# Optimization experiments

Hardware: AMD Instinct MI355X
Metric: run time of the kernel (lower is better)

## Reference

```python
import jax, jax.numpy as jnp
import numpy as np

H = 1024
S = 32768

def setup_inputs() -> dict:
    key = jax.random.key(0)
    ks = jax.random.split(key, 6)
    scale = 1.0 / np.sqrt(H)
    return {
        "hidden": jax.random.normal(ks[0], (H,), dtype=jnp.float32),
        "encoder_states": jax.random.normal(ks[1], (S, H), dtype=jnp.float32),
        "W_lin": jax.random.normal(ks[2], (H, H), dtype=jnp.float32) * scale,
        "b_lin": jax.random.normal(ks[3], (H,), dtype=jnp.float32) * scale,
        "W_attn": jax.random.normal(ks[4], (H, H), dtype=jnp.float32) * scale,
        "b_attn": jax.random.normal(ks[5], (H,), dtype=jnp.float32) * scale,
    }

def reference(hidden, encoder_states, W_lin, b_lin, W_attn, b_attn):
    # hidden = self.linear(hidden)  (torch Linear: x @ W.T + b)
    h = jnp.dot(W_lin, hidden) + b_lin               # [H]
    # 'general' score: energy = attn(hidden); e_i = enc_i . energy
    energy = jnp.dot(W_attn, h) + b_attn             # [H]
    attn_energies = encoder_states @ energy          # [S]  (vectorized GEMV over all timesteps)
    return jax.nn.softmax(attn_energies, axis=0)[:, None]  # [S, 1]
```

## Files before the change

### kernel.cpp

```cpp
#include <hip/hip_runtime.h>
#include <math.h>

#define H 1024
#define S 32768

__device__ __forceinline__ float wave_reduce_sum(float v) {
    #pragma unroll
    for (int off = 32; off > 0; off >>= 1) v += __shfl_xor(v, off, 64);
    return v;
}

__global__ __launch_bounds__(256) void gemv_kernel(const float* __restrict__ W,
                                                   const float* __restrict__ x,
                                                   const float* __restrict__ b,
                                                   float* __restrict__ y) {
    __shared__ float xs[H];
    const int tid = threadIdx.x;
    reinterpret_cast<float4*>(xs)[tid] = reinterpret_cast<const float4*>(x)[tid];
    __syncthreads();

    const int wave = tid >> 6, lane = tid & 63;
    const int row = blockIdx.x * 4 + wave;
    const float4* Wr = reinterpret_cast<const float4*>(W + (size_t)row * H);
    const float4* xs4 = reinterpret_cast<const float4*>(xs);

    float acc = 0.f;
    #pragma unroll
    for (int k = 0; k < 4; ++k) {
        const int idx = k * 64 + lane;
        const float4 w = Wr[idx];
        const float4 e = xs4[idx];
        acc += w.x * e.x + w.y * e.y + w.z * e.z + w.w * e.w;
    }
    acc = wave_reduce_sum(acc);
    if (lane == 0) y[row] = acc + b[row];
}

__global__ __launch_bounds__(256) void scores_kernel(const float* __restrict__ enc,
                                                     const float* __restrict__ energy,
                                                     float* __restrict__ scores,
                                                     float* __restrict__ blockmax) {
    __shared__ float es[H];
    __shared__ float smax[4];
    const int tid = threadIdx.x;
    reinterpret_cast<float4*>(es)[tid] = reinterpret_cast<const float4*>(energy)[tid];
    __syncthreads();

    const int wave = tid >> 6, lane = tid & 63;
    const int row = blockIdx.x * 4 + wave;
    const float4* Er = reinterpret_cast<const float4*>(enc + (size_t)row * H);
    const float4* es4 = reinterpret_cast<const float4*>(es);

    float acc = 0.f;
    #pragma unroll
    for (int k = 0; k < 4; ++k) {
        const int idx = k * 64 + lane;
        const float4 w = Er[idx];
        const float4 e = es4[idx];
        acc += w.x * e.x + w.y * e.y + w.z * e.z + w.w * e.w;
    }
    acc = wave_reduce_sum(acc);
    if (lane == 0) { scores[row] = acc; smax[wave] = acc; }
    __syncthreads();
    if (tid == 0) {
        blockmax[blockIdx.x] = fmaxf(fmaxf(smax[0], smax[1]), fmaxf(smax[2], smax[3]));
    }
}

__global__ __launch_bounds__(1024) void softmax_reduce_kernel(const float* __restrict__ scores,
                                                              const float* __restrict__ blockmax,
                                                              int nbm,
                                                              float* __restrict__ stats) {
    __shared__ float red[1024];
    const int tid = threadIdx.x;

    float m = -INFINITY;
    for (int i = tid; i < nbm; i += 1024) m = fmaxf(m, blockmax[i]);
    red[tid] = m;
    __syncthreads();
    for (int s = 512; s > 0; s >>= 1) {
        if (tid < s) red[tid] = fmaxf(red[tid], red[tid + s]);
        __syncthreads();
    }
    m = red[0];
    __syncthreads();

    float sum = 0.f;
    for (int i = tid; i < S; i += 1024) sum += expf(scores[i] - m);
    red[tid] = sum;
    __syncthreads();
    for (int s = 512; s > 0; s >>= 1) {
        if (tid < s) red[tid] += red[tid + s];
        __syncthreads();
    }
    if (tid == 0) { stats[0] = m; stats[1] = 1.0f / red[0]; }
}

__global__ __launch_bounds__(256) void normalize_kernel(const float* __restrict__ scores,
                                                        const float* __restrict__ stats,
                                                        float* __restrict__ out) {
    const int i = blockIdx.x * 256 + threadIdx.x;
    const float m = stats[0], inv = stats[1];
    out[i] = expf(scores[i] - m) * inv;
}

extern "C" void kernel_launch(void* const* d_in, const int* in_sizes, int n_in,
                              void* d_out, int out_size, void* d_ws, size_t ws_size,
                              hipStream_t stream) {
    const float* hidden = (const float*)d_in[0];
    const float* enc    = (const float*)d_in[1];
    const float* W_lin  = (const float*)d_in[2];
    const float* b_lin  = (const float*)d_in[3];
    const float* W_attn = (const float*)d_in[4];
    const float* b_attn = (const float*)d_in[5];
    float* out = (float*)d_out;
    float* ws  = (float*)d_ws;

    float* scores   = ws;
    float* blockmax = ws + S;
    float* h        = ws + S + 8192;
    float* energy   = ws + S + 8192 + H;
    float* stats    = ws + S + 8192 + 2*H;

    const int nblk_scores = S / 4;

    gemv_kernel<<<H / 4, 256, 0, stream>>>(W_lin, hidden, b_lin, h);
    gemv_kernel<<<H / 4, 256, 0, stream>>>(W_attn, h, b_attn, energy);
    scores_kernel<<<nblk_scores, 256, 0, stream>>>(enc, energy, scores, blockmax);
    softmax_reduce_kernel<<<1, 1024, 0, stream>>>(scores, blockmax, nblk_scores, stats);
    normalize_kernel<<<S / 256, 256, 0, stream>>>(scores, stats, out);
}
```

Measured before the change: 221.4 us.

## Fuse scores, softmax reduction and normalization via last-block atomic counter

Merges the scores GEMV, the softmax statistics reduction and the normalization into one kernel. Each block computes four rows per wave, a local max and a rescaled exp-sum. The last block to finish, detected with an atomic counter reset by the first GEMV, combines the per-block statistics and writes the normalized output. This removes two kernel launches and the single-block pass that recomputed exp over all scores. The trade-off is that the final normalization runs on only one block of 256 threads, which serializes that tail.

```diff
diff --git a/kernel.cpp b/kernel.cpp
--- a/kernel.cpp
+++ b/kernel.cpp
@@ -3,6 +3,7 @@
 
 #define H 1024
 #define S 32768
+#define NB3 2048
 
 __device__ __forceinline__ float wave_reduce_sum(float v) {
     #pragma unroll
@@ -13,95 +14,126 @@
 __global__ __launch_bounds__(256) void gemv_kernel(const float* __restrict__ W,
                                                    const float* __restrict__ x,
                                                    const float* __restrict__ b,
-                                                   float* __restrict__ y) {
+                                                   float* __restrict__ y,
+                                                   unsigned int* counter) {
     __shared__ float xs[H];
     const int tid = threadIdx.x;
+    if (counter && blockIdx.x == 0 && tid == 0) *counter = 0u;
     reinterpret_cast<float4*>(xs)[tid] = reinterpret_cast<const float4*>(x)[tid];
     __syncthreads();
 
     const int wave = tid >> 6, lane = tid & 63;
     const int row = blockIdx.x * 4 + wave;
-    const float4* Wr = reinterpret_cast<const float4*>(W + (size_t)row * H);
+    const float4* Wr  = reinterpret_cast<const float4*>(W + (size_t)row * H);
     const float4* xs4 = reinterpret_cast<const float4*>(xs);
 
     float acc = 0.f;
     #pragma unroll
     for (int k = 0; k < 4; ++k) {
-        const int idx = k * 64 + lane;
-        const float4 w = Wr[idx];
-        const float4 e = xs4[idx];
+        const float4 w = Wr[k * 64 + lane];
+        const float4 e = xs4[k * 64 + lane];
         acc += w.x * e.x + w.y * e.y + w.z * e.z + w.w * e.w;
     }
     acc = wave_reduce_sum(acc);
     if (lane == 0) y[row] = acc + b[row];
 }
 
-__global__ __launch_bounds__(256) void scores_kernel(const float* __restrict__ enc,
-                                                     const float* __restrict__ energy,
-                                                     float* __restrict__ scores,
-                                                     float* __restrict__ blockmax) {
+__global__ __launch_bounds__(256) void scores_softmax_kernel(
+    const float* __restrict__ enc,
+    const float* __restrict__ energy,
+    float* __restrict__ scores,
+    float* __restrict__ blockmax,
+    float* __restrict__ blocksum,
+    unsigned int* __restrict__ counter,
+    float* __restrict__ out)
+{
     __shared__ float es[H];
-    __shared__ float smax[4];
+    __shared__ float redm[4], reds[4];
+    __shared__ unsigned int isLast;
+
     const int tid = threadIdx.x;
     reinterpret_cast<float4*>(es)[tid] = reinterpret_cast<const float4*>(energy)[tid];
     __syncthreads();
 
     const int wave = tid >> 6, lane = tid & 63;
-    const int row = blockIdx.x * 4 + wave;
-    const float4* Er = reinterpret_cast<const float4*>(enc + (size_t)row * H);
+    const int bid  = blockIdx.x;
     const float4* es4 = reinterpret_cast<const float4*>(es);
 
-    float acc = 0.f;
+    const int wrow0 = (bid * 4 + wave) * 4;
+    float sc[4];
+    float wmax = -INFINITY;
     #pragma unroll
-    for (int k = 0; k < 4; ++k) {
-        const int idx = k * 64 + lane;
-        const float4 w = Er[idx];
-        const float4 e = es4[idx];
-        acc += w.x * e.x + w.y * e.y + w.z * e.z + w.w * e.w;
+    for (int p = 0; p < 4; ++p) {
+        const float4* Er = reinterpret_cast<const float4*>(enc + (size_t)(wrow0 + p) * H);
+        float acc = 0.f;
+        #pragma unroll
+        for (int k = 0; k < 4; ++k) {
+            const float4 w = Er[k * 64 + lane];
+            const float4 e = es4[k * 64 + lane];
+            acc += w.x * e.x + w.y * e.y + w.z * e.z + w.w * e.w;
+        }
+        acc = wave_reduce_sum(acc);
+        sc[p] = acc;
+        wmax = fmaxf(wmax, acc);
     }
-    acc = wave_reduce_sum(acc);
-    if (lane == 0) { scores[row] = acc; smax[wave] = acc; }
+    if (lane == 0) {
+        reinterpret_cast<float4*>(scores)[bid * 4 + wave] =
+            make_float4(sc[0], sc[1], sc[2], sc[3]);
+        redm[wave] = wmax;
+    }
+    __syncthreads();
+    const float bm = fmaxf(fmaxf(redm[0], redm[1]), fmaxf(redm[2], redm[3]));
+
+    float wsum = 0.f;
+    #pragma unroll
+    for (int p = 0; p < 4; ++p) wsum += expf(sc[p] - bm);
+    if (lane == 0) reds[wave] = wsum;
     __syncthreads();
     if (tid == 0) {
-        blockmax[blockIdx.x] = fmaxf(fmaxf(smax[0], smax[1]), fmaxf(smax[2], smax[3]));
+        blockmax[bid] = bm;
+        blocksum[bid] = reds[0] + reds[1] + reds[2] + reds[3];
     }
-}
 
-__global__ __launch_bounds__(1024) void softmax_reduce_kernel(const float* __restrict__ scores,
-                                                              const float* __restrict__ blockmax,
-                                                              int nbm,
-                                                              float* __restrict__ stats) {
-    __shared__ float red[1024];
-    const int tid = threadIdx.x;
+    __threadfence();
+    if (tid == 0) isLast = (atomicAdd(counter, 1u) == (unsigned)(gridDim.x - 1));
+    __syncthreads();
+    if (!isLast) return;
+    __threadfence();
 
+    __shared__ float fred[256];
     float m = -INFINITY;
-    for (int i = tid; i < nbm; i += 1024) m = fmaxf(m, blockmax[i]);
-    red[tid] = m;
+    #pragma unroll
+    for (int i = 0; i < NB3 / 256; ++i) m = fmaxf(m, blockmax[tid + i * 256]);
+    fred[tid] = m;
     __syncthreads();
-    for (int s = 512; s > 0; s >>= 1) {
-        if (tid < s) red[tid] = fmaxf(red[tid], red[tid + s]);
+    for (int s = 128; s > 0; s >>= 1) {
+        if (tid < s) fred[tid] = fmaxf(fred[tid], fred[tid + s]);
         __syncthreads();
     }
-    m = red[0];
+    const float M = fred[0];
     __syncthreads();
 
-    float sum = 0.f;
-    for (int i = tid; i < S; i += 1024) sum += expf(scores[i] - m);
-    red[tid] = sum;
+    float t = 0.f;
+    #pragma unroll
+    for (int i = 0; i < NB3 / 256; ++i) {
+        const int b = tid + i * 256;
+        t += blocksum[b] * expf(blockmax[b] - M);
+    }
+    fred[tid] = t;
     __syncthreads();
-    for (int s = 512; s > 0; s >>= 1) {
-        if (tid < s) red[tid] += red[tid + s];
+    for (int s = 128; s > 0; s >>= 1) {
+        if (tid < s) fred[tid] += fred[tid + s];
         __syncthreads();
     }
-    if (tid == 0) { stats[0] = m; stats[1] = 1.0f / red[0]; }
-}
+    const float inv = 1.0f / fred[0];
 
-__global__ __launch_bounds__(256) void normalize_kernel(const float* __restrict__ scores,
-                                                        const float* __restrict__ stats,
-                                                        float* __restrict__ out) {
-    const int i = blockIdx.x * 256 + threadIdx.x;
-    const float m = stats[0], inv = stats[1];
-    out[i] = expf(scores[i] - m) * inv;
+    const float4* s4 = reinterpret_cast<const float4*>(scores);
+    float4* o4 = reinterpret_cast<float4*>(out);
+    for (int i = tid; i < S / 4; i += 256) {
+        const float4 v = s4[i];
+        o4[i] = make_float4(expf(v.x - M) * inv, expf(v.y - M) * inv,
+                            expf(v.z - M) * inv, expf(v.w - M) * inv);
+    }
 }
 
 extern "C" void kernel_launch(void* const* d_in, const int* in_sizes, int n_in,
@@ -118,15 +150,13 @@
 
     float* scores   = ws;
     float* blockmax = ws + S;
-    float* h        = ws + S + 8192;
-    float* energy   = ws + S + 8192 + H;
-    float* stats    = ws + S + 8192 + 2*H;
+    float* blocksum = ws + S + NB3;
+    float* h        = ws + S + 2 * NB3;
+    float* energy   = ws + S + 2 * NB3 + H;
+    unsigned int* counter = (unsigned int*)(ws + S + 2 * NB3 + 2 * H);
 
-    const int nblk_scores = S / 4;
-
-    gemv_kernel<<<H / 4, 256, 0, stream>>>(W_lin, hidden, b_lin, h);
-    gemv_kernel<<<H / 4, 256, 0, stream>>>(W_attn, h, b_attn, energy);
-    scores_kernel<<<nblk_scores, 256, 0, stream>>>(enc, energy, scores, blockmax);
-    softmax_reduce_kernel<<<1, 1024, 0, stream>>>(scores, blockmax, nblk_scores, stats);
-    normalize_kernel<<<S / 256, 256, 0, stream>>>(scores, stats, out);
+    gemv_kernel<<<H / 4, 256, 0, stream>>>(W_lin, hidden, b_lin, h, counter);
+    gemv_kernel<<<H / 4, 256, 0, stream>>>(W_attn, h, b_attn, energy, nullptr);
+    scores_softmax_kernel<<<NB3, 256, 0, stream>>>(enc, energy, scores, blockmax,
+                                                   blocksum, counter, out);
 }
```

New measurement: 593.6 us. 2.68x slower.
